# Kernel tuning notes

Measured on AMD Instinct MI355X. Metric: run time of the kernel, lower is better.

## Reference

```python
import jax, jax.numpy as jnp
import numpy as np

EMBED_DIM = 1024
NUM_HEADS = 16
HEAD_DIM = EMBED_DIM // NUM_HEADS


def setup_inputs() -> dict:
    key = jax.random.key(0)
    ks = jax.random.split(key, 5)
    B, S, D = 2, 2048, EMBED_DIM
    scale = 1.0 / np.sqrt(D)
    x = jax.random.normal(ks[0], (B, S, D), dtype=jnp.float32)
    W_qkv = jax.random.normal(ks[1], (D, 3 * D), dtype=jnp.float32) * scale
    b_qkv = jnp.zeros((3 * D,), dtype=jnp.float32)
    W_out = jax.random.normal(ks[2], (D, D), dtype=jnp.float32) * scale
    b_out = jnp.zeros((D,), dtype=jnp.float32)
    return {"x": x, "W_qkv": W_qkv, "b_qkv": b_qkv, "W_out": W_out, "b_out": b_out}


def reference(x, W_qkv, b_qkv, W_out, b_out):
    B, S, D = x.shape
    H, Hd = NUM_HEADS, HEAD_DIM
    qkv = x @ W_qkv + b_qkv                       # [B,S,3D]
    qkv = qkv.reshape(B, S, 3, H, Hd)
    q = qkv[:, :, 0].transpose(0, 2, 1, 3)        # [B,H,S,Hd]
    k = qkv[:, :, 1].transpose(0, 2, 1, 3)
    v = qkv[:, :, 2].transpose(0, 2, 1, 3)
    scores = jnp.einsum('bhqd,bhkd->bhqk', q, k) / np.sqrt(Hd)  # [B,H,S,S]
    causal = jnp.tril(jnp.ones((S, S), dtype=bool))
    scores = jnp.where(causal[None, None], scores, -jnp.inf)
    attn = jax.nn.softmax(scores, axis=-1)
    out = jnp.einsum('bhqk,bhkd->bhqd', attn, v)  # [B,H,S,Hd]
    out = out.transpose(0, 2, 1, 3).reshape(B, S, D)
    return out @ W_out + b_out
```

## Files before the change

kernel.cpp:

```cpp
#include <hip/hip_runtime.h>
#include <hip/hip_bf16.h>
#include <math.h>

#define EMBED_DIM 1024
#define NUM_HEADS 16
#define HEAD_DIM 64
#define BATCH 2
#define SEQ 2048

using short8  = __attribute__((ext_vector_type(8))) short;
using floatx4 = __attribute__((ext_vector_type(4))) float;

__device__ __forceinline__ ushort f2bf(float f) {
    unsigned u = __float_as_uint(f);
    u = (u + 0x7FFFu + ((u >> 16) & 1u)) >> 16;
    return (ushort)u;
}

__device__ __forceinline__ unsigned bfpack2(float a, float b) {
    return ((__float_as_uint(a) + 0x8000u) >> 16) |
           (((__float_as_uint(b) + 0x8000u) >> 16) << 16);
}

__device__ __forceinline__ void load_lds16(const ushort* g, ushort* l) {
    __builtin_amdgcn_global_load_lds(
        (const __attribute__((address_space(1))) void*)g,
        (__attribute__((address_space(3))) void*)l, 16, 0, 0);
}

__device__ __forceinline__ void tc_tile(
    const float* __restrict__ W, ushort* __restrict__ Wt,
    int K, int N, int n0, int k0, float (*t)[65])
{
    const int c = threadIdx.x & 63, r0 = (threadIdx.x >> 6) * 16;
    #pragma unroll
    for (int r = 0; r < 16; ++r)
        t[r0 + r][c] = W[(size_t)(k0 + r0 + r) * N + n0 + c];
    __syncthreads();
    #pragma unroll
    for (int r = 0; r < 16; ++r)
        Wt[(size_t)(n0 + r0 + r) * K + k0 + c] = f2bf(t[c][r0 + r]);
}

__global__ __launch_bounds__(256) void prep_all(
    const float* __restrict__ x, const float* __restrict__ W_qkv,
    const float* __restrict__ W_out,
    ushort* __restrict__ xb, ushort* __restrict__ Wqb_t, ushort* __restrict__ Wob_t)
{
    __shared__ float t[64][65];
    const int bx = blockIdx.x;
    if (bx < 4096) {
        int i = (bx * 256 + threadIdx.x) * 4;
        float4 v = *(const float4*)&x[i];
        ushort4 o = { f2bf(v.x), f2bf(v.y), f2bf(v.z), f2bf(v.w) };
        *(ushort4*)&xb[i] = o;
    } else if (bx < 4096 + 768) {
        int b = bx - 4096;
        tc_tile(W_qkv, Wqb_t, 1024, 3072, (b % 48) * 64, (b / 48) * 64, t);
    } else {
        int b = bx - 4864;
        tc_tile(W_out, Wob_t, 1024, 1024, (b % 16) * 64, (b / 16) * 64, t);
    }
}

#define GK 1024

__device__ __forceinline__ void gemm_core(
    const ushort* __restrict__ A, const ushort* __restrict__ Bt,
    int m0, int n0, ushort* As, ushort* Bs, floatx4 acc[4][4])
{
    const int tid  = threadIdx.x;
    const int w    = tid >> 6;
    const int lane = tid & 63;
    const int col  = lane & 15;
    const int quad = lane >> 4;
    const int wm   = w >> 1, wn = w & 1;

    #pragma unroll
    for (int i = 0; i < 4; ++i)
        #pragma unroll
        for (int j = 0; j < 4; ++j)
            acc[i][j] = (floatx4){0.f, 0.f, 0.f, 0.f};

    const int o0   = w * 2048 + lane * 16;
    const int row0 = o0 >> 6;
    const int ke0  = (o0 & 63) >> 1;

    for (int k0 = 0; k0 < GK; k0 += 32) {
        #pragma unroll
        for (int t = 0; t < 2; ++t) {
            const int row = row0 + t * 16;
            ushort* la = As + ((w * 2048 + t * 1024) >> 1);
            ushort* lb = Bs + ((w * 2048 + t * 1024) >> 1);
            load_lds16(A  + (size_t)(m0 + row) * GK + k0 + ke0, la);
            load_lds16(Bt + (size_t)(n0 + row) * GK + k0 + ke0, lb);
        }
        __syncthreads();

        short8 af[4], bf[4];
        #pragma unroll
        for (int i = 0; i < 4; ++i)
            af[i] = *(const short8*)&As[(wm * 64 + i * 16 + col) * 32 + quad * 8];
        #pragma unroll
        for (int j = 0; j < 4; ++j)
            bf[j] = *(const short8*)&Bs[(wn * 64 + j * 16 + col) * 32 + quad * 8];
        #pragma unroll
        for (int i = 0; i < 4; ++i)
            #pragma unroll
            for (int j = 0; j < 4; ++j)
                acc[i][j] = __builtin_amdgcn_mfma_f32_16x16x32_bf16(af[i], bf[j], acc[i][j], 0, 0, 0);

        __syncthreads();
    }
}

__global__ __launch_bounds__(256) void gemm_qkv_mfma(
    const ushort* __restrict__ A, const ushort* __restrict__ Bt,
    const float* __restrict__ bias,
    ushort* __restrict__ Qb, ushort* __restrict__ Kb, ushort* __restrict__ Vt)
{
    __shared__ __align__(16) ushort As[128 * 32];
    __shared__ __align__(16) ushort Bs[128 * 32];
    const int n0 = blockIdx.x * 128;
    const int m0 = blockIdx.y * 128;

    floatx4 acc[4][4];
    gemm_core(A, Bt, m0, n0, As, Bs, acc);

    const int lane = threadIdx.x & 63;
    const int w    = threadIdx.x >> 6;
    const int col  = lane & 15, quad = lane >> 4;
    const int wm   = w >> 1, wn = w & 1;

    #pragma unroll
    for (int j = 0; j < 4; ++j) {
        const int n = n0 + wn * 64 + j * 16 + col;
        const float bj = bias[n];
        const int part = n >> 10;
        const int h = (n >> 6) & 15;
        const int d = n & 63;
        #pragma unroll
        for (int i = 0; i < 4; ++i)
            #pragma unroll
            for (int r = 0; r < 4; ++r) {
                const int m = m0 + wm * 64 + i * 16 + quad * 4 + r;
                const int b = m >> 11, s = m & 2047;
                const int bh = b * 16 + h;
                const ushort bv = f2bf(acc[i][j][r] + bj);
                if (part == 0)      Qb[((size_t)bh * SEQ + s) * 64 + d] = bv;
                else if (part == 1) Kb[((size_t)bh * SEQ + s) * 64 + d] = bv;
                else                Vt[((size_t)bh * 64 + d) * SEQ + s] = bv;
            }
    }
}

__global__ __launch_bounds__(256) void gemm_out_mfma(
    const ushort* __restrict__ A, const ushort* __restrict__ Bt,
    const float* __restrict__ bias, float* __restrict__ out)
{
    __shared__ __align__(16) ushort As[128 * 32];
    __shared__ __align__(16) ushort Bs[128 * 32];
    const int n0 = blockIdx.x * 128;
    const int m0 = blockIdx.y * 128;

    floatx4 acc[4][4];
    gemm_core(A, Bt, m0, n0, As, Bs, acc);

    const int lane = threadIdx.x & 63;
    const int w    = threadIdx.x >> 6;
    const int col  = lane & 15, quad = lane >> 4;
    const int wm   = w >> 1, wn = w & 1;

    #pragma unroll
    for (int j = 0; j < 4; ++j) {
        const int n = n0 + wn * 64 + j * 16 + col;
        const float bj = bias[n];
        #pragma unroll
        for (int i = 0; i < 4; ++i)
            #pragma unroll
            for (int r = 0; r < 4; ++r) {
                const int m = m0 + wm * 64 + i * 16 + quad * 4 + r;
                out[(size_t)m * EMBED_DIM + n] = acc[i][j][r] + bj;
            }
    }
}

#define LP 72

__global__ __launch_bounds__(256) void attn_fused(
    const ushort* __restrict__ Qb, const ushort* __restrict__ Kb,
    const ushort* __restrict__ Vt, ushort* __restrict__ out)
{
    const int id = blockIdx.x;
    const int qt = 31 - (id >> 5);
    const int bh = id & 31;
    const int b  = bh >> 4, h = bh & 15;
    const int q0 = qt * 64;

    __shared__ __align__(16) ushort Qs[8 * 512];
    __shared__ __align__(16) ushort Ks[8 * 512];
    __shared__ __align__(16) ushort Vs[8 * 512];
    __shared__ __align__(16) ushort Ps[64 * LP];
    __shared__ __align__(16) float  ls[4][16];

    const int tid  = threadIdx.x;
    const int w    = tid >> 6;
    const int lane = tid & 63;
    const int col  = lane & 15;
    const int quad = lane >> 4;

    {
        const ushort* Qg = Qb + ((size_t)bh * SEQ + q0) * 64;
        #pragma unroll
        for (int t = 0; t < 2; ++t) {
            const ushort* g = Qg + (size_t)(w * 16 + col) * 64 + t * 32 + quad * 8;
            load_lds16(g, &Qs[(w * 2 + t) * 512]);
        }
    }

    const ushort* kg[2];
    const ushort* vg[2];
    #pragma unroll
    for (int t = 0; t < 2; ++t) {
        kg[t] = Kb + (size_t)bh * SEQ * 64 + (size_t)(w * 16 + col) * 64 + t * 32 + quad * 8;
        vg[t] = Vt + (size_t)bh * 64 * SEQ + (size_t)(w * 16 + col) * SEQ + t * 32 + quad * 8;
    }

    __syncthreads();
    const short8 a0 = *(const short8*)&Qs[(w * 2 + 0) * 512 + lane * 8];
    const short8 a1 = *(const short8*)&Qs[(w * 2 + 1) * 512 + lane * 8];

    floatx4 acc_o[4];
    #pragma unroll
    for (int dbi = 0; dbi < 4; ++dbi) acc_o[dbi] = (floatx4){0.f, 0.f, 0.f, 0.f};
    float l_lane = 0.f;

    const int myq = w * 16 + col;

    for (int kt = 0; kt <= qt; ++kt) {
        __syncthreads();
        #pragma unroll
        for (int t = 0; t < 2; ++t) {
            load_lds16(kg[t], &Ks[(w * 2 + t) * 512]);
            load_lds16(vg[t], &Vs[(w * 2 + t) * 512]);
            kg[t] += 64 * 64;
            vg[t] += 64;
        }
        __syncthreads();

        floatx4 s_acc[4];
        #pragma unroll
        for (int kb = 0; kb < 4; ++kb) {
            short8 k0f = *(const short8*)&Ks[(kb * 2 + 0) * 512 + lane * 8];
            short8 k1f = *(const short8*)&Ks[(kb * 2 + 1) * 512 + lane * 8];
            floatx4 z = (floatx4){0.f, 0.f, 0.f, 0.f};
            z = __builtin_amdgcn_mfma_f32_16x16x32_bf16(k0f, a0, z, 0, 0, 0);
            z = __builtin_amdgcn_mfma_f32_16x16x32_bf16(k1f, a1, z, 0, 0, 0);
            s_acc[kb] = z;
        }

        if (kt == qt) {
            #pragma unroll
            for (int kb = 0; kb < 4; ++kb) {
                const int kbase = kb * 16 + quad * 4;
                float p[4];
                #pragma unroll
                for (int r = 0; r < 4; ++r) {
                    float e = __expf(s_acc[kb][r] * 0.125f);
                    p[r] = (kbase + r > myq) ? 0.f : e;
                    l_lane += p[r];
                }
                uint2 u = { bfpack2(p[0], p[1]), bfpack2(p[2], p[3]) };
                *(uint2*)&Ps[myq * LP + kbase] = u;
            }
        } else {
            #pragma unroll
            for (int kb = 0; kb < 4; ++kb) {
                const int kbase = kb * 16 + quad * 4;
                float p[4];
                #pragma unroll
                for (int r = 0; r < 4; ++r) {
                    p[r] = __expf(s_acc[kb][r] * 0.125f);
                    l_lane += p[r];
                }
                uint2 u = { bfpack2(p[0], p[1]), bfpack2(p[2], p[3]) };
                *(uint2*)&Ps[myq * LP + kbase] = u;
            }
        }

        short8 pa0 = *(const short8*)&Ps[(w * 16 + col) * LP + quad * 8];
        short8 pa1 = *(const short8*)&Ps[(w * 16 + col) * LP + 32 + quad * 8];
        #pragma unroll
        for (int dbi = 0; dbi < 4; ++dbi) {
            short8 vb0 = *(const short8*)&Vs[(dbi * 2 + 0) * 512 + lane * 8];
            short8 vb1 = *(const short8*)&Vs[(dbi * 2 + 1) * 512 + lane * 8];
            acc_o[dbi] = __builtin_amdgcn_mfma_f32_16x16x32_bf16(pa0, vb0, acc_o[dbi], 0, 0, 0);
            acc_o[dbi] = __builtin_amdgcn_mfma_f32_16x16x32_bf16(pa1, vb1, acc_o[dbi], 0, 0, 0);
        }
    }

    l_lane += __shfl_xor(l_lane, 16);
    l_lane += __shfl_xor(l_lane, 32);
    if (quad == 0) ls[w][col] = 1.f / l_lane;
    float4 invv = *(const float4*)&ls[w][quad * 4];

    #pragma unroll
    for (int dbi = 0; dbi < 4; ++dbi)
        #pragma unroll
        for (int r = 0; r < 4; ++r) {
            int q = q0 + w * 16 + quad * 4 + r;
            int d = dbi * 16 + col;
            float inv = (r == 0) ? invv.x : (r == 1) ? invv.y : (r == 2) ? invv.z : invv.w;
            out[((size_t)(b * SEQ + q)) * EMBED_DIM + h * 64 + d] = f2bf(acc_o[dbi][r] * inv);
        }
}

extern "C" void kernel_launch(void* const* d_in, const int* in_sizes, int n_in,
                              void* d_out, int out_size, void* d_ws, size_t ws_size,
                              hipStream_t stream)
{
    const float* x     = (const float*)d_in[0];
    const float* W_qkv = (const float*)d_in[1];
    const float* b_qkv = (const float*)d_in[2];
    const float* W_out = (const float*)d_in[3];
    const float* b_out = (const float*)d_in[4];
    float* out = (float*)d_out;

    const int M  = BATCH * SEQ;
    const int D  = EMBED_DIM;
    const int N1 = 3 * D;
    const size_t HE = (size_t)BATCH * NUM_HEADS * SEQ * 64;

    ushort* xb    = (ushort*)d_ws;
    ushort* Wqb_t = xb + (size_t)M * D;
    ushort* Wob_t = Wqb_t + (size_t)D * N1;
    ushort* Qb    = Wob_t + (size_t)D * D;
    ushort* Kb    = Qb + HE;
    ushort* Vt    = Kb + HE;
    ushort* attnb = Vt + HE;

    prep_all<<<5120, 256, 0, stream>>>(x, W_qkv, W_out, xb, Wqb_t, Wob_t);

    gemm_qkv_mfma<<<dim3(N1 / 128, M / 128), 256, 0, stream>>>(
        xb, Wqb_t, b_qkv, Qb, Kb, Vt);

    attn_fused<<<dim3(32 * 32), 256, 0, stream>>>(Qb, Kb, Vt, attnb);

    gemm_out_mfma<<<dim3(D / 128, M / 128), 256, 0, stream>>>(
        attnb, Wob_t, b_out, out);
}
```

Baseline: 195.9 us.

## Double-buffer LDS tiles in GEMMs and attention to overlap loads with MFMA

Adds ping-pong LDS buffers to the shared GEMM core and to the attention K/V tiles. The next tile is prefetched while the current one is consumed, and the loop drops to one barrier per iteration. This is meant to hide global-to-LDS load latency behind matrix math, at the cost of doubled LDS footprint and possibly lower occupancy.

```diff
diff --git a/kernel.cpp b/kernel.cpp
--- a/kernel.cpp
+++ b/kernel.cpp
@@ -67,7 +67,8 @@
 
 __device__ __forceinline__ void gemm_core(
     const ushort* __restrict__ A, const ushort* __restrict__ Bt,
-    int m0, int n0, ushort* As, ushort* Bs, floatx4 acc[4][4])
+    int m0, int n0, ushort* As0, ushort* As1, ushort* Bs0, ushort* Bs1,
+    floatx4 acc[4][4])
 {
     const int tid  = threadIdx.x;
     const int w    = tid >> 6;
@@ -85,25 +86,40 @@
     const int o0   = w * 2048 + lane * 16;
     const int row0 = o0 >> 6;
     const int ke0  = (o0 & 63) >> 1;
+    const int loff = (w * 2048) >> 1;
+
+    const ushort* ga = A  + (size_t)(m0 + row0) * GK + ke0;
+    const ushort* gb = Bt + (size_t)(n0 + row0) * GK + ke0;
+
+    #pragma unroll
+    for (int t = 0; t < 2; ++t) {
+        load_lds16(ga + (size_t)t * 16 * GK, As0 + loff + t * 512);
+        load_lds16(gb + (size_t)t * 16 * GK, Bs0 + loff + t * 512);
+    }
+    __syncthreads();
 
     for (int k0 = 0; k0 < GK; k0 += 32) {
-        #pragma unroll
-        for (int t = 0; t < 2; ++t) {
-            const int row = row0 + t * 16;
-            ushort* la = As + ((w * 2048 + t * 1024) >> 1);
-            ushort* lb = Bs + ((w * 2048 + t * 1024) >> 1);
-            load_lds16(A  + (size_t)(m0 + row) * GK + k0 + ke0, la);
-            load_lds16(Bt + (size_t)(n0 + row) * GK + k0 + ke0, lb);
-        }
-        __syncthreads();
+        const int cur = (k0 >> 5) & 1;
+        ushort* Ac = cur ? As1 : As0;
+        ushort* Bc = cur ? Bs1 : Bs0;
+        ushort* An = cur ? As0 : As1;
+        ushort* Bn = cur ? Bs0 : Bs1;
+
+        if (k0 + 32 < GK) {
+            #pragma unroll
+            for (int t = 0; t < 2; ++t) {
+                load_lds16(ga + (k0 + 32) + (size_t)t * 16 * GK, An + loff + t * 512);
+                load_lds16(gb + (k0 + 32) + (size_t)t * 16 * GK, Bn + loff + t * 512);
+            }
+        }
 
         short8 af[4], bf[4];
         #pragma unroll
         for (int i = 0; i < 4; ++i)
-            af[i] = *(const short8*)&As[(wm * 64 + i * 16 + col) * 32 + quad * 8];
+            af[i] = *(const short8*)&Ac[(wm * 64 + i * 16 + col) * 32 + quad * 8];
         #pragma unroll
         for (int j = 0; j < 4; ++j)
-            bf[j] = *(const short8*)&Bs[(wn * 64 + j * 16 + col) * 32 + quad * 8];
+            bf[j] = *(const short8*)&Bc[(wn * 64 + j * 16 + col) * 32 + quad * 8];
         #pragma unroll
         for (int i = 0; i < 4; ++i)
             #pragma unroll
@@ -119,13 +135,13 @@
     const float* __restrict__ bias,
     ushort* __restrict__ Qb, ushort* __restrict__ Kb, ushort* __restrict__ Vt)
 {
-    __shared__ __align__(16) ushort As[128 * 32];
-    __shared__ __align__(16) ushort Bs[128 * 32];
+    __shared__ __align__(16) ushort As[2][128 * 32];
+    __shared__ __align__(16) ushort Bs[2][128 * 32];
     const int n0 = blockIdx.x * 128;
     const int m0 = blockIdx.y * 128;
 
     floatx4 acc[4][4];
-    gemm_core(A, Bt, m0, n0, As, Bs, acc);
+    gemm_core(A, Bt, m0, n0, As[0], As[1], Bs[0], Bs[1], acc);
 
     const int lane = threadIdx.x & 63;
     const int w    = threadIdx.x >> 6;
@@ -158,13 +174,13 @@
     const ushort* __restrict__ A, const ushort* __restrict__ Bt,
     const float* __restrict__ bias, float* __restrict__ out)
 {
-    __shared__ __align__(16) ushort As[128 * 32];
-    __shared__ __align__(16) ushort Bs[128 * 32];
+    __shared__ __align__(16) ushort As[2][128 * 32];
+    __shared__ __align__(16) ushort Bs[2][128 * 32];
     const int n0 = blockIdx.x * 128;
     const int m0 = blockIdx.y * 128;
 
     floatx4 acc[4][4];
-    gemm_core(A, Bt, m0, n0, As, Bs, acc);
+    gemm_core(A, Bt, m0, n0, As[0], As[1], Bs[0], Bs[1], acc);
 
     const int lane = threadIdx.x & 63;
     const int w    = threadIdx.x >> 6;
@@ -198,8 +214,8 @@
     const int q0 = qt * 64;
 
     __shared__ __align__(16) ushort Qs[8 * 512];
-    __shared__ __align__(16) ushort Ks[8 * 512];
-    __shared__ __align__(16) ushort Vs[8 * 512];
+    __shared__ __align__(16) ushort Ks[2][8 * 512];
+    __shared__ __align__(16) ushort Vs[2][8 * 512];
     __shared__ __align__(16) ushort Ps[64 * LP];
     __shared__ __align__(16) float  ls[4][16];
 
@@ -209,15 +225,6 @@
     const int col  = lane & 15;
     const int quad = lane >> 4;
 
-    {
-        const ushort* Qg = Qb + ((size_t)bh * SEQ + q0) * 64;
-        #pragma unroll
-        for (int t = 0; t < 2; ++t) {
-            const ushort* g = Qg + (size_t)(w * 16 + col) * 64 + t * 32 + quad * 8;
-            load_lds16(g, &Qs[(w * 2 + t) * 512]);
-        }
-    }
-
     const ushort* kg[2];
     const ushort* vg[2];
     #pragma unroll
@@ -226,7 +233,20 @@
         vg[t] = Vt + (size_t)bh * 64 * SEQ + (size_t)(w * 16 + col) * SEQ + t * 32 + quad * 8;
     }
 
+    {
+        const ushort* Qg = Qb + ((size_t)bh * SEQ + q0) * 64;
+        #pragma unroll
+        for (int t = 0; t < 2; ++t) {
+            load_lds16(Qg + (size_t)(w * 16 + col) * 64 + t * 32 + quad * 8,
+                       &Qs[(w * 2 + t) * 512]);
+            load_lds16(kg[t], &Ks[0][(w * 2 + t) * 512]);
+            load_lds16(vg[t], &Vs[0][(w * 2 + t) * 512]);
+            kg[t] += 64 * 64;
+            vg[t] += 64;
+        }
+    }
     __syncthreads();
+
     const short8 a0 = *(const short8*)&Qs[(w * 2 + 0) * 512 + lane * 8];
     const short8 a1 = *(const short8*)&Qs[(w * 2 + 1) * 512 + lane * 8];
 
@@ -234,25 +254,30 @@
     #pragma unroll
     for (int dbi = 0; dbi < 4; ++dbi) acc_o[dbi] = (floatx4){0.f, 0.f, 0.f, 0.f};
     float l_lane = 0.f;
-
     const int myq = w * 16 + col;
 
     for (int kt = 0; kt <= qt; ++kt) {
-        __syncthreads();
-        #pragma unroll
-        for (int t = 0; t < 2; ++t) {
-            load_lds16(kg[t], &Ks[(w * 2 + t) * 512]);
-            load_lds16(vg[t], &Vs[(w * 2 + t) * 512]);
-            kg[t] += 64 * 64;
-            vg[t] += 64;
-        }
-        __syncthreads();
+        const int cur = kt & 1;
+        const ushort* Kc = Ks[cur];
+        const ushort* Vc = Vs[cur];
+
+        if (kt < qt) {
+            ushort* Kn = (ushort*)Ks[cur ^ 1];
+            ushort* Vn = (ushort*)Vs[cur ^ 1];
+            #pragma unroll
+            for (int t = 0; t < 2; ++t) {
+                load_lds16(kg[t], &Kn[(w * 2 + t) * 512]);
+                load_lds16(vg[t], &Vn[(w * 2 + t) * 512]);
+                kg[t] += 64 * 64;
+                vg[t] += 64;
+            }
+        }
 
         floatx4 s_acc[4];
         #pragma unroll
         for (int kb = 0; kb < 4; ++kb) {
-            short8 k0f = *(const short8*)&Ks[(kb * 2 + 0) * 512 + lane * 8];
-            short8 k1f = *(const short8*)&Ks[(kb * 2 + 1) * 512 + lane * 8];
+            short8 k0f = *(const short8*)&Kc[(kb * 2 + 0) * 512 + lane * 8];
+            short8 k1f = *(const short8*)&Kc[(kb * 2 + 1) * 512 + lane * 8];
             floatx4 z = (floatx4){0.f, 0.f, 0.f, 0.f};
             z = __builtin_amdgcn_mfma_f32_16x16x32_bf16(k0f, a0, z, 0, 0, 0);
             z = __builtin_amdgcn_mfma_f32_16x16x32_bf16(k1f, a1, z, 0, 0, 0);
@@ -292,11 +317,13 @@
         short8 pa1 = *(const short8*)&Ps[(w * 16 + col) * LP + 32 + quad * 8];
         #pragma unroll
         for (int dbi = 0; dbi < 4; ++dbi) {
-            short8 vb0 = *(const short8*)&Vs[(dbi * 2 + 0) * 512 + lane * 8];
-            short8 vb1 = *(const short8*)&Vs[(dbi * 2 + 1) * 512 + lane * 8];
+            short8 vb0 = *(const short8*)&Vc[(dbi * 2 + 0) * 512 + lane * 8];
+            short8 vb1 = *(const short8*)&Vc[(dbi * 2 + 1) * 512 + lane * 8];
             acc_o[dbi] = __builtin_amdgcn_mfma_f32_16x16x32_bf16(pa0, vb0, acc_o[dbi], 0, 0, 0);
             acc_o[dbi] = __builtin_amdgcn_mfma_f32_16x16x32_bf16(pa1, vb1, acc_o[dbi], 0, 0, 0);
         }
+
+        __syncthreads();
     }
 
     l_lane += __shfl_xor(l_lane, 16);
```

After: 191.2 us. 2.4% less time.
